# Performance work log

Measured on AMD Instinct MI355X. Metric: run time of the kernel, lower is better.

## Reference

```python
import jax, jax.numpy as jnp
import numpy as np

BN_EPS = 1e-5

# Binary activation with hardtanh STE semantics (forward: sign)
@jax.custom_vjp
def binary_act(x):
    return jnp.sign(x)

def _ba_fwd(x):
    return jnp.sign(x), x

def _ba_bwd(x, g):
    return (jnp.where(jnp.abs(x) > 1.0, 0.0, g),)

binary_act.defvjp(_ba_fwd, _ba_bwd)

# Binary weight quantizer (forward: sign, backward: identity STE)
@jax.custom_vjp
def binary_w(x):
    return jnp.sign(x)

def _bw_fwd(x):
    return jnp.sign(x), None

def _bw_bwd(_, g):
    return (g,)

binary_w.defvjp(_bw_fwd, _bw_bwd)


def setup_inputs() -> dict:
    key = jax.random.key(0)
    k1, k2, k3 = jax.random.split(key, 3)
    B, C_in, H, W_sp = 32, 256, 56, 56
    C_out, KH, KW = 256, 3, 3
    x = jax.random.normal(k1, (B, C_in, H, W_sp), dtype=jnp.float32)
    weight = jax.random.normal(k2, (C_out, C_in, KH, KW), dtype=jnp.float32) * 0.05
    bias = jax.random.normal(k3, (C_out,), dtype=jnp.float32) * 0.01
    gamma = jnp.ones((C_out,), dtype=jnp.float32)
    beta = jnp.zeros((C_out,), dtype=jnp.float32)
    return {"x": x, "weight": weight, "bias": bias, "gamma": gamma, "beta": beta}


def reference(x, weight, bias, gamma, beta):
    # --- activation binarization (A=2): sign ---
    xb = binary_act(x)
    # --- weight binarization (W=2): mean-center over in-channel dim, clamp, sign * alpha ---
    wc = weight - jnp.mean(weight, axis=1, keepdims=True)
    wc = jnp.clip(wc, -1.0, 1.0)
    alpha = jnp.mean(jnp.abs(wc), axis=(1, 2, 3), keepdims=True)  # per-output-channel scale
    wq = binary_w(wc) * alpha
    # --- conv2d, stride 1, padding 1 ---
    y = jax.lax.conv_general_dilated(
        xb, wq, window_strides=(1, 1), padding=((1, 1), (1, 1)),
        dimension_numbers=("NCHW", "OIHW", "NCHW"))
    y = y + bias[None, :, None, None]
    # --- BatchNorm2d (training-mode batch statistics, biased variance) ---
    mu = jnp.mean(y, axis=(0, 2, 3), keepdims=True)
    var = jnp.var(y, axis=(0, 2, 3), keepdims=True)
    y = (y - mu) * jax.lax.rsqrt(var + BN_EPS)
    y = y * gamma[None, :, None, None] + beta[None, :, None, None]
    # --- last_relu=1 ---
    y = jax.nn.relu(y)
    # --- last_bin=1 (A=2 -> binary activation) ---
    y = binary_act(y)
    return y
```

## Files before the change

### kernel.cpp

```cpp
#include <hip/hip_runtime.h>

typedef unsigned long long u64;
typedef int i32x4 __attribute__((ext_vector_type(4)));
typedef int i32x16 __attribute__((ext_vector_type(16)));
typedef short s16x8 __attribute__((ext_vector_type(8)));
typedef float f32x4 __attribute__((ext_vector_type(4)));

#define N_SP 3136
#define C_IN 256
#define C_OUT 256
#define BATCH 32
#define NBLK 1792
#define XROW 64
#define XPLANE (58 * XROW * 256)
#define XSIZE ((size_t)BATCH * XPLANE)
#define S16_OFF ((size_t)36 << 20)
#define S16_BYTES ((size_t)BATCH * C_OUT * N_SP * 2)

__global__ __launch_bounds__(256) void prep_weights(const float* __restrict__ w,
                                                    char* __restrict__ A_pack,
                                                    double* __restrict__ alpha) {
    const int o = blockIdx.x;
    const int i = threadIdx.x;
    const int lane = i & 63, wvid = i >> 6;
    __shared__ double part[4][9];
    __shared__ double part2[4];

    float wv[9];
    const float* wp = w + ((size_t)o * C_IN + i) * 9;
#pragma unroll
    for (int t = 0; t < 9; ++t) wv[t] = wp[t];

#pragma unroll
    for (int t = 0; t < 9; ++t) {
        double v = (double)wv[t];
#pragma unroll
        for (int off = 32; off > 0; off >>= 1) v += __shfl_down(v, off);
        if (lane == 0) part[wvid][t] = v;
    }
    __syncthreads();

    double asum = 0.0;
#pragma unroll
    for (int t = 0; t < 9; ++t) {
        double mean = (part[0][t] + part[1][t] + part[2][t] + part[3][t]) * (1.0 / 256.0);
        double wc = (double)wv[t] - mean;
        int idx16 = ((t * 8 + (i >> 5)) * 8 + (o >> 5)) * 64 + (((i >> 4) & 1) << 5) + (o & 31);
        A_pack[(size_t)idx16 * 16 + (i & 15)] = (char)(wc > 0.0 ? 1 : -1);
        double aw = fabs(wc);
        if (aw > 1.0) aw = 1.0;
        asum += aw;
    }
#pragma unroll
    for (int off = 32; off > 0; off >>= 1) asum += __shfl_down(asum, off);
    if (lane == 0) part2[wvid] = asum;
    __syncthreads();
    if (i == 0)
        alpha[o] = (part2[0] + part2[1] + part2[2] + part2[3]) * (1.0 / 2304.0);
}

__global__ __launch_bounds__(256) void sign_transpose(const float* __restrict__ x,
                                                      char* __restrict__ xsT) {
    const int sp0 = blockIdx.x * 64;
    const int b = blockIdx.y;
    const int lane = threadIdx.x & 63;
    const int wv = threadIdx.x >> 6;
    __shared__ char tile[64 * 272];

    {
        const int tidl = (blockIdx.y * 49 + blockIdx.x) * 256 + threadIdx.x;
        if (tidl < 294912) {
            const int bb = tidl / 9216;
            const int r = tidl - bb * 9216;
            int hp, wp, c16;
            if (r < 2048) {
                hp = (r >> 10) * 57;
                wp = (r >> 4) & 63;
                c16 = (r & 15) << 4;
            } else {
                int r2 = r - 2048;
                hp = 1 + (r2 >> 7);
                int q = r2 & 127;
                int wi = q >> 4;
                wp = (wi == 0) ? 0 : 56 + wi;
                c16 = (q & 15) << 4;
            }
            *(i32x4*)(xsT + (((size_t)(bb * 58 + hp) << 6) + wp) * 256 + c16) =
                (i32x4){0, 0, 0, 0};
        }
    }

    const float* xp = x + ((size_t)(b * 256 + (wv << 6))) * N_SP + sp0 + lane;
#pragma unroll
    for (int q = 0; q < 4; ++q) {
        unsigned d[4];
#pragma unroll
        for (int dd = 0; dd < 4; ++dd) {
            unsigned v = 0;
#pragma unroll
            for (int kk = 0; kk < 4; ++kk) {
                int ci_l = (q << 4) + (dd << 2) + kk;
                float xv = __builtin_nontemporal_load(xp + (size_t)ci_l * N_SP);
                v |= (unsigned)(xv > 0.0f ? 0x01u : 0xFFu) << (8 * kk);
            }
            d[dd] = v;
        }
        *(i32x4*)(tile + lane * 272 + (wv << 6) + (q << 4)) =
            (i32x4){(int)d[0], (int)d[1], (int)d[2], (int)d[3]};
    }
    __syncthreads();

    const int t = threadIdx.x;
#pragma unroll
    for (int j = 0; j < 4; ++j) {
        int sp_loc = (j << 4) + (t >> 4);
        int ci0 = (t & 15) << 4;
        i32x4 v = *(const i32x4*)(tile + sp_loc * 272 + ci0);
        int spg = sp0 + sp_loc;
        int h = spg / 56, w = spg - h * 56;
        size_t dst = (((size_t)(b * 58 + h + 1) << 6) + (w + 1)) * 256 + ci0;
        *(i32x4*)(xsT + dst) = v;
    }
}

__global__ __launch_bounds__(512, 4) void conv_mfma(const char* __restrict__ xsT,
                                                    const char* __restrict__ A_pack,
                                                    float* __restrict__ out,
                                                    short* __restrict__ s16,
                                                    int2* __restrict__ partials) {
    const int tid = threadIdx.x;
    const int lane = tid & 63;
    const int wv = tid >> 6;
    const int l31 = lane & 31, l5 = lane >> 5;
    const int blk = blockIdx.x;
    const int b = blk / 56;
    const int h0 = blk - b * 56;

    __shared__ char slab[3 * 58 * 272];

    {
        const char* src = xsT + ((size_t)(b * 58 + h0) << 6) * 256;
        for (int c = tid; c < 3 * 58 * 16; c += 512) {
            int dh = c / (58 * 16);
            int rem = c - dh * (58 * 16);
            int wp = rem >> 4, c16 = (rem & 15) << 4;
            *(i32x4*)(slab + (dh * 58 + wp) * 272 + c16) =
                *(const i32x4*)(src + (size_t)dh * (XROW * 256) + wp * 256 + c16);
        }
    }
    __syncthreads();

    i32x16 acc[2] = {};

    const char* apb = A_pack + (size_t)(wv * 1024) + lane * 16;
    const char* sb0 = slab + l31 * 272 + l5 * 16;
    int w1_0 = 32 + l31;     if (w1_0 > 57) w1_0 = 57;
    int w1_1 = 33 + l31;     if (w1_1 > 57) w1_1 = 57;
    int w1_2 = 34 + l31;     if (w1_2 > 57) w1_2 = 57;
    const char* sb1_0 = slab + w1_0 * 272 + l5 * 16;
    const char* sb1_1 = slab + w1_1 * 272 + l5 * 16;
    const char* sb1_2 = slab + w1_2 * 272 + l5 * 16;

#pragma unroll
    for (int tap = 0; tap < 9; ++tap) {
        const int dh = tap / 3, dw = tap - 3 * (tap / 3);
        const char* sb1 = (dw == 0) ? sb1_0 : ((dw == 1) ? sb1_1 : sb1_2);
#pragma unroll
        for (int cib = 0; cib < 8; ++cib) {
            const int it = tap * 8 + cib;
            i32x4 a = *(const i32x4*)(apb + (size_t)it * 8192);
            i32x4 b0 = *(const i32x4*)(sb0 + (dh * 58 + dw) * 272 + cib * 32);
            i32x4 b1 = *(const i32x4*)(sb1 + dh * 58 * 272 + cib * 32);
            acc[0] = __builtin_amdgcn_mfma_i32_32x32x32_i8(a, b0, acc[0], 0, 0, 0);
            acc[1] = __builtin_amdgcn_mfma_i32_32x32x32_i8(a, b1, acc[1], 0, 0, 0);
        }
    }

    if (s16) {
        short* sb = s16 + ((size_t)(b * 256 + wv * 32)) * N_SP + h0 * 56;
#pragma unroll
        for (int nh = 0; nh < 2; ++nh) {
            const int w = nh * 32 + l31;
            if (w < 56) {
#pragma unroll
                for (int reg = 0; reg < 16; ++reg) {
                    int corow = (reg & 3) + 8 * (reg >> 2) + 4 * l5;
                    __builtin_nontemporal_store(
                        (short)acc[nh][reg],
                        sb + (size_t)corow * N_SP + w);
                }
            }
        }
    } else {
        float* ob = out + ((size_t)(b * 256 + wv * 32)) * N_SP + h0 * 56;
#pragma unroll
        for (int nh = 0; nh < 2; ++nh) {
            const int w = nh * 32 + l31;
            if (w < 56) {
#pragma unroll
                for (int reg = 0; reg < 16; ++reg) {
                    int corow = (reg & 3) + 8 * (reg >> 2) + 4 * l5;
                    __builtin_nontemporal_store(
                        (float)acc[nh][reg],
                        ob + (size_t)corow * N_SP + w);
                }
            }
        }
    }

    __syncthreads();
    int* sp_s = (int*)slab;
    int* sp_q = (int*)slab + 256;
#pragma unroll
    for (int reg = 0; reg < 16; ++reg) {
        int v0 = acc[0][reg];
        int v1 = (l31 < 24) ? acc[1][reg] : 0;
        int s = v0 + v1;
        unsigned q = (unsigned)(v0 * v0) + (unsigned)(v1 * v1);
#pragma unroll
        for (int off = 16; off > 0; off >>= 1) {
            s += __shfl_xor(s, off);
            q += (unsigned)__shfl_xor((int)q, off);
        }
        if (l31 == 0) {
            int corow = (reg & 3) + 8 * (reg >> 2) + 4 * l5;
            sp_s[wv * 32 + corow] = s;
            sp_q[wv * 32 + corow] = (int)q;
        }
    }
    __syncthreads();
    if (tid < 256) {
        u64 v = (u64)(unsigned)sp_s[tid] | ((u64)(unsigned)sp_q[tid] << 32);
        __builtin_nontemporal_store(v, (u64*)(partials + (size_t)tid * NBLK + blk));
    }
}

__global__ __launch_bounds__(256) void stats_consts(const int2* __restrict__ partials,
                                                    const double* __restrict__ alpha,
                                                    const float* __restrict__ gamma,
                                                    const float* __restrict__ beta,
                                                    double* __restrict__ AB) {
    const int c = blockIdx.x;
    const int t = threadIdx.x;
    long long s1 = 0, s2 = 0;
    for (int blk = t; blk < NBLK; blk += 256) {
        int2 v = partials[(size_t)c * NBLK + blk];
        s1 += v.x;
        s2 += (long long)v.y;
    }
#pragma unroll
    for (int off = 32; off > 0; off >>= 1) {
        s1 += __shfl_down(s1, off);
        s2 += __shfl_down(s2, off);
    }
    __shared__ long long p1[4], p2[4];
    if ((t & 63) == 0) { p1[t >> 6] = s1; p2[t >> 6] = s2; }
    __syncthreads();
    if (t == 0) {
        double S1 = (double)(p1[0] + p1[1] + p1[2] + p1[3]);
        double S2 = (double)(p2[0] + p2[1] + p2[2] + p2[3]);
        const double N = (double)(BATCH * N_SP);
        double mu = S1 / N;
        double var = S2 / N - mu * mu;
        double a = alpha[c];
        double vy = a * a * var;
        double scale = (double)gamma[c] / sqrt(vy + 1e-5);
        double A = a * scale;
        double B = (double)beta[c] - A * mu;
        AB[c] = A;
        AB[C_OUT + c] = B;
    }
}

__global__ __launch_bounds__(256) void finalize(float* __restrict__ out,
                                                const double* __restrict__ AB) {
    const unsigned i4 = blockIdx.x * 256 + threadIdx.x;
    const unsigned e = i4 << 2;
    const int c = (int)((e / N_SP) & (C_OUT - 1));
    const double A = AB[c];
    const double B = AB[C_OUT + c];
    float4 v = ((float4*)out)[i4];
    v.x = (A * (double)v.x + B) > 0.0 ? 1.0f : 0.0f;
    v.y = (A * (double)v.y + B) > 0.0 ? 1.0f : 0.0f;
    v.z = (A * (double)v.z + B) > 0.0 ? 1.0f : 0.0f;
    v.w = (A * (double)v.w + B) > 0.0 ? 1.0f : 0.0f;
    ((float4*)out)[i4] = v;
}

__global__ __launch_bounds__(256) void finalize16(const short* __restrict__ S,
                                                  float* __restrict__ out,
                                                  const double* __restrict__ AB) {
    const unsigned t = blockIdx.x * 256 + threadIdx.x;
    const unsigned e = t << 3;
    const int c = (int)((e / N_SP) & (C_OUT - 1));
    const double A = AB[c];
    const double B = AB[C_OUT + c];
    s16x8 v = __builtin_nontemporal_load((const s16x8*)(S + e));
    f32x4 o0, o1;
    o0.x = (A * (double)v[0] + B) > 0.0 ? 1.0f : 0.0f;
    o0.y = (A * (double)v[1] + B) > 0.0 ? 1.0f : 0.0f;
    o0.z = (A * (double)v[2] + B) > 0.0 ? 1.0f : 0.0f;
    o0.w = (A * (double)v[3] + B) > 0.0 ? 1.0f : 0.0f;
    o1.x = (A * (double)v[4] + B) > 0.0 ? 1.0f : 0.0f;
    o1.y = (A * (double)v[5] + B) > 0.0 ? 1.0f : 0.0f;
    o1.z = (A * (double)v[6] + B) > 0.0 ? 1.0f : 0.0f;
    o1.w = (A * (double)v[7] + B) > 0.0 ? 1.0f : 0.0f;
    __builtin_nontemporal_store(o0, (f32x4*)(out + e));
    __builtin_nontemporal_store(o1, (f32x4*)(out + e + 4));
}

extern "C" void kernel_launch(void* const* d_in, const int* in_sizes, int n_in,
                              void* d_out, int out_size, void* d_ws, size_t ws_size,
                              hipStream_t stream) {
    const float* x      = (const float*)d_in[0];
    const float* weight = (const float*)d_in[1];
    const float* bias   = (const float*)d_in[2];   (void)bias;
    const float* gamma  = (const float*)d_in[3];
    const float* beta   = (const float*)d_in[4];
    float* out = (float*)d_out;

    char* ws = (char*)d_ws;
    double* alpha = (double*)(ws + 4096);
    double* AB    = (double*)(ws + 8192);
    char*   A_pack = (char*)(ws + 16384);
    int2*   partials = (int2*)(ws + (1 << 20));
    char*   xsT   = (char*)(ws + (5 << 20));
    const bool use16 = ws_size >= S16_OFF + S16_BYTES;
    short*  s16 = use16 ? (short*)(ws + S16_OFF) : (short*)0;

    prep_weights<<<C_OUT, 256, 0, stream>>>(weight, A_pack, alpha);
    sign_transpose<<<dim3(49, BATCH), 256, 0, stream>>>(x, xsT);
    conv_mfma<<<dim3(NBLK), 512, 0, stream>>>(xsT, A_pack, out, s16, partials);
    stats_consts<<<C_OUT, 256, 0, stream>>>(partials, alpha, gamma, beta, AB);
    if (use16)
        finalize16<<<12544, 256, 0, stream>>>(s16, out, AB);
    else
        finalize<<<(out_size / 4) / 256, 256, 0, stream>>>(out, AB);
}
```

Baseline: 307.6 us.

## Merge weight prep into sign-transpose kernel and vectorize activation loads

Combines the weight binarization kernel and the activation sign/transpose kernel into one launch, with block ranges dispatched by block index, which removes one kernel launch and lets the two independent jobs run concurrently. The activation path now reads float4 vectors across four spatial positions per thread instead of scalar loads per channel, which cuts the number of load instructions. It also treats the sum-of-squares partial as unsigned so large per-block values are not sign-extended. The cost is more LDS per block from the union of shared arrays, plus a shared-memory write pattern that may cause more bank conflicts.

```diff
diff --git a/kernel.cpp b/kernel.cpp
--- a/kernel.cpp
+++ b/kernel.cpp
@@ -17,108 +17,119 @@
 #define S16_OFF ((size_t)36 << 20)
 #define S16_BYTES ((size_t)BATCH * C_OUT * N_SP * 2)
 
-__global__ __launch_bounds__(256) void prep_weights(const float* __restrict__ w,
-                                                    char* __restrict__ A_pack,
-                                                    double* __restrict__ alpha) {
-    const int o = blockIdx.x;
-    const int i = threadIdx.x;
-    const int lane = i & 63, wvid = i >> 6;
-    __shared__ double part[4][9];
-    __shared__ double part2[4];
-
-    float wv[9];
-    const float* wp = w + ((size_t)o * C_IN + i) * 9;
-#pragma unroll
-    for (int t = 0; t < 9; ++t) wv[t] = wp[t];
-
-#pragma unroll
-    for (int t = 0; t < 9; ++t) {
-        double v = (double)wv[t];
-#pragma unroll
-        for (int off = 32; off > 0; off >>= 1) v += __shfl_down(v, off);
-        if (lane == 0) part[wvid][t] = v;
-    }
-    __syncthreads();
-
-    double asum = 0.0;
-#pragma unroll
-    for (int t = 0; t < 9; ++t) {
-        double mean = (part[0][t] + part[1][t] + part[2][t] + part[3][t]) * (1.0 / 256.0);
-        double wc = (double)wv[t] - mean;
-        int idx16 = ((t * 8 + (i >> 5)) * 8 + (o >> 5)) * 64 + (((i >> 4) & 1) << 5) + (o & 31);
-        A_pack[(size_t)idx16 * 16 + (i & 15)] = (char)(wc > 0.0 ? 1 : -1);
-        double aw = fabs(wc);
-        if (aw > 1.0) aw = 1.0;
-        asum += aw;
-    }
-#pragma unroll
-    for (int off = 32; off > 0; off >>= 1) asum += __shfl_down(asum, off);
-    if (lane == 0) part2[wvid] = asum;
-    __syncthreads();
-    if (i == 0)
-        alpha[o] = (part2[0] + part2[1] + part2[2] + part2[3]) * (1.0 / 2304.0);
-}
-
-__global__ __launch_bounds__(256) void sign_transpose(const float* __restrict__ x,
-                                                      char* __restrict__ xsT) {
-    const int sp0 = blockIdx.x * 64;
-    const int b = blockIdx.y;
-    const int lane = threadIdx.x & 63;
-    const int wv = threadIdx.x >> 6;
+__global__ __launch_bounds__(256) void prep_and_transpose(const float* __restrict__ x,
+                                                          char* __restrict__ xsT,
+                                                          const float* __restrict__ w,
+                                                          char* __restrict__ A_pack,
+                                                          double* __restrict__ alpha) {
+    const int bid = blockIdx.x;
+    const int t = threadIdx.x;
+
+    if (bid >= 1568) {
+        const int o = bid - 1568;
+        const int i = t;
+        const int lane = i & 63, wvid = i >> 6;
+        __shared__ double part[4][9];
+        __shared__ double part2[4];
+
+        float wv[9];
+        const float* wp = w + ((size_t)o * C_IN + i) * 9;
+#pragma unroll
+        for (int tt = 0; tt < 9; ++tt) wv[tt] = wp[tt];
+
+#pragma unroll
+        for (int tt = 0; tt < 9; ++tt) {
+            double v = (double)wv[tt];
+#pragma unroll
+            for (int off = 32; off > 0; off >>= 1) v += __shfl_down(v, off);
+            if (lane == 0) part[wvid][tt] = v;
+        }
+        __syncthreads();
+
+        double asum = 0.0;
+#pragma unroll
+        for (int tt = 0; tt < 9; ++tt) {
+            double mean = (part[0][tt] + part[1][tt] + part[2][tt] + part[3][tt]) * (1.0 / 256.0);
+            double wc = (double)wv[tt] - mean;
+            int idx16 = ((tt * 8 + (i >> 5)) * 8 + (o >> 5)) * 64 + (((i >> 4) & 1) << 5) + (o & 31);
+            A_pack[(size_t)idx16 * 16 + (i & 15)] = (char)(wc > 0.0 ? 1 : -1);
+            double aw = fabs(wc);
+            if (aw > 1.0) aw = 1.0;
+            asum += aw;
+        }
+#pragma unroll
+        for (int off = 32; off > 0; off >>= 1) asum += __shfl_down(asum, off);
+        if (lane == 0) part2[wvid] = asum;
+        __syncthreads();
+        if (i == 0)
+            alpha[o] = (part2[0] + part2[1] + part2[2] + part2[3]) * (1.0 / 2304.0);
+        return;
+    }
+
+    const int b = bid / 49;
+    const int sp0 = (bid - b * 49) * 64;
     __shared__ char tile[64 * 272];
 
     {
-        const int tidl = (blockIdx.y * 49 + blockIdx.x) * 256 + threadIdx.x;
+        const int tidl = bid * 256 + t;
         if (tidl < 294912) {
             const int bb = tidl / 9216;
             const int r = tidl - bb * 9216;
-            int hp, wp, c16;
+            int hp, wp2, c16;
             if (r < 2048) {
                 hp = (r >> 10) * 57;
-                wp = (r >> 4) & 63;
+                wp2 = (r >> 4) & 63;
                 c16 = (r & 15) << 4;
             } else {
                 int r2 = r - 2048;
                 hp = 1 + (r2 >> 7);
                 int q = r2 & 127;
                 int wi = q >> 4;
-                wp = (wi == 0) ? 0 : 56 + wi;
+                wp2 = (wi == 0) ? 0 : 56 + wi;
                 c16 = (q & 15) << 4;
             }
-            *(i32x4*)(xsT + (((size_t)(bb * 58 + hp) << 6) + wp) * 256 + c16) =
+            *(i32x4*)(xsT + (((size_t)(bb * 58 + hp) << 6) + wp2) * 256 + c16) =
                 (i32x4){0, 0, 0, 0};
         }
     }
 
-    const float* xp = x + ((size_t)(b * 256 + (wv << 6))) * N_SP + sp0 + lane;
-#pragma unroll
-    for (int q = 0; q < 4; ++q) {
-        unsigned d[4];
-#pragma unroll
-        for (int dd = 0; dd < 4; ++dd) {
-            unsigned v = 0;
-#pragma unroll
-            for (int kk = 0; kk < 4; ++kk) {
-                int ci_l = (q << 4) + (dd << 2) + kk;
-                float xv = __builtin_nontemporal_load(xp + (size_t)ci_l * N_SP);
-                v |= (unsigned)(xv > 0.0f ? 0x01u : 0xFFu) << (8 * kk);
-            }
-            d[dd] = v;
-        }
-        *(i32x4*)(tile + lane * 272 + (wv << 6) + (q << 4)) =
-            (i32x4){(int)d[0], (int)d[1], (int)d[2], (int)d[3]};
-    }
-    __syncthreads();
-
-    const int t = threadIdx.x;
+    const int wv = t >> 6;
+    const int lane = t & 63;
+    const int sq = lane & 15;
+    const int cg = lane >> 4;
+    const int ci0t = wv * 64 + cg * 16;
+
+    unsigned d[4][4];
+#pragma unroll
+    for (int j = 0; j < 4; ++j)
+#pragma unroll
+        for (int ww = 0; ww < 4; ++ww) d[j][ww] = 0;
+
+    const float* xp = x + ((size_t)(b * 256 + ci0t)) * N_SP + sp0 + sq * 4;
+#pragma unroll
+    for (int k = 0; k < 16; ++k) {
+        f32x4 v = __builtin_nontemporal_load((const f32x4*)(xp + (size_t)k * N_SP));
+        const int ww = k >> 2, sh = (k & 3) * 8;
+        d[0][ww] |= (v[0] > 0.0f ? 0x01u : 0xFFu) << sh;
+        d[1][ww] |= (v[1] > 0.0f ? 0x01u : 0xFFu) << sh;
+        d[2][ww] |= (v[2] > 0.0f ? 0x01u : 0xFFu) << sh;
+        d[3][ww] |= (v[3] > 0.0f ? 0x01u : 0xFFu) << sh;
+    }
+#pragma unroll
+    for (int j = 0; j < 4; ++j) {
+        *(i32x4*)(tile + (sq * 4 + j) * 272 + ci0t) =
+            (i32x4){(int)d[j][0], (int)d[j][1], (int)d[j][2], (int)d[j][3]};
+    }
+    __syncthreads();
+
 #pragma unroll
     for (int j = 0; j < 4; ++j) {
         int sp_loc = (j << 4) + (t >> 4);
         int ci0 = (t & 15) << 4;
         i32x4 v = *(const i32x4*)(tile + sp_loc * 272 + ci0);
         int spg = sp0 + sp_loc;
-        int h = spg / 56, w = spg - h * 56;
-        size_t dst = (((size_t)(b * 58 + h + 1) << 6) + (w + 1)) * 256 + ci0;
+        int h = spg / 56, w2 = spg - h * 56;
+        size_t dst = (((size_t)(b * 58 + h + 1) << 6) + (w2 + 1)) * 256 + ci0;
         *(i32x4*)(xsT + dst) = v;
     }
 }
@@ -246,7 +257,7 @@
     for (int blk = t; blk < NBLK; blk += 256) {
         int2 v = partials[(size_t)c * NBLK + blk];
         s1 += v.x;
-        s2 += (long long)v.y;
+        s2 += (long long)(unsigned)v.y;
     }
 #pragma unroll
     for (int off = 32; off > 0; off >>= 1) {
@@ -328,8 +339,7 @@
     const bool use16 = ws_size >= S16_OFF + S16_BYTES;
     short*  s16 = use16 ? (short*)(ws + S16_OFF) : (short*)0;
 
-    prep_weights<<<C_OUT, 256, 0, stream>>>(weight, A_pack, alpha);
-    sign_transpose<<<dim3(49, BATCH), 256, 0, stream>>>(x, xsT);
+    prep_and_transpose<<<1824, 256, 0, stream>>>(x, xsT, weight, A_pack, alpha);
     conv_mfma<<<dim3(NBLK), 512, 0, stream>>>(xsT, A_pack, out, s16, partials);
     stats_consts<<<C_OUT, 256, 0, stream>>>(partials, alpha, gamma, beta, AB);
     if (use16)
```

New measurement: 302.1 us. No clear change (-1.8%).
